# Kernel tuning notes

Measured on AMD Instinct MI355X. Metric: run time of the kernel, lower is better.

Reference implementation:

```python
import jax, jax.numpy as jnp
import numpy as np

EPS = 1e-16


def setup_inputs() -> dict:
    key = jax.random.key(0)
    k1, k2 = jax.random.split(key)
    p = jax.random.normal(k1, (2, 32, 2048, 4), dtype=jnp.float32)
    q = jax.random.normal(k2, (32, 2048, 4), dtype=jnp.float32)
    return {"p": p, "q": q}


def reference(p, q):
    # im=False path: take the real part of the complex generated momenta
    p_real = p[0]                      # (B, N, 4)
    # loss_norm_choice='p3', take_sqrt=True: use 3-momenta (drop energy)
    p3 = p_real[..., 1:]               # (B, N, 3)
    q3 = q[..., 1:]                    # (B, M, 3)
    # Pairwise Euclidean distance (cdist) via the expanded quadratic form to
    # avoid materializing the (B, N, M, 3) difference tensor.
    x2 = jnp.sum(p3 * p3, axis=-1)     # (B, N)
    y2 = jnp.sum(q3 * q3, axis=-1)     # (B, M)
    xy = jnp.einsum('bnd,bmd->bnm', p3, q3)  # (B, N, M)
    dist_sq = x2[..., :, None] + y2[..., None, :] - 2.0 * xy
    dist = jnp.sqrt(jnp.maximum(dist_sq, 0.0) + EPS)  # (B, N, M)
    # Bidirectional nearest-neighbor min-reduction
    min_pq = jnp.min(dist, axis=-1)    # (B, N)
    min_qp = jnp.min(dist, axis=-2)    # (B, M)
    chamfer_loss = jnp.sum((min_pq + min_qp) * 0.5)
    return chamfer_loss
```

## Files before the change

kernel.cpp:

```cpp
#include <hip/hip_runtime.h>
#include <math.h>


#define NPTS   2048
#define NBATCH 32
#define BROWS  128
#define BCOLS  512
#define NBI    (NPTS / BROWS)
#define NJC    (NPTS / BCOLS)
#define WS_ROW_FLOATS ((size_t)NBATCH * NBI * NJC * BROWS)
#define EPSF   1e-16f
#define BIGF   3.4e38f
#define ONEBF  0x3F80u

typedef __attribute__((ext_vector_type(8))) short bf16x8;
typedef __attribute__((ext_vector_type(4))) float f32x4;
typedef __attribute__((ext_vector_type(4))) unsigned int u32x4;

__device__ __forceinline__ float min3f(float a, float b, float c) {
    return fminf(fminf(a, b), c);
}
__device__ __forceinline__ unsigned short bf16_rne(float f) {
    unsigned int u = __float_as_uint(f);
    return (unsigned short)((u + 0x7FFFu + ((u >> 16) & 1u)) >> 16);
}
__device__ __forceinline__ float bf16_f32(unsigned short h) {
    return __uint_as_float(((unsigned int)h) << 16);
}

__global__ __launch_bounds__(256, 4) void chamfer_mfma_kernel(
    const float* __restrict__ P, const float* __restrict__ Q,
    float* __restrict__ ws, float* __restrict__ out)
{
    __shared__ u32x4        sB0[BCOLS];
    __shared__ u32x4        sB1[BCOLS];
    __shared__ u32x4        sB2[BCOLS];
    __shared__ unsigned int scol[BCOLS];
    __shared__ float        srow[BROWS];

    const int tid  = threadIdx.x;
    const int lane = tid & 63;
    const int wv   = tid >> 6;
    const int c15  = lane & 15;
    const int g    = lane >> 4;
    const int bi   = blockIdx.x;
    const int jc   = blockIdx.y;
    const int b    = blockIdx.z;

    if (bi == 0 && jc == 0 && b == 0 && tid == 0) *out = 0.f;

    {
        const float4* Qb = (const float4*)Q + (size_t)b * NPTS + jc * BCOLS;
        #pragma unroll
        for (int s = 0; s < 2; ++s) {
            int c = tid + 256 * s;
            float4 qv = Qb[c];
            float gx = -2.f * qv.y, gy = -2.f * qv.z, gz = -2.f * qv.w;
            unsigned short hx = bf16_rne(gx), hy = bf16_rne(gy), hz = bf16_rne(gz);
            unsigned short lx = bf16_rne(gx - bf16_f32(hx));
            unsigned short ly = bf16_rne(gy - bf16_f32(hy));
            unsigned short lz = bf16_rne(gz - bf16_f32(hz));
            float y2 = fmaf(qv.y, qv.y, fmaf(qv.z, qv.z, qv.w * qv.w));
            unsigned short y2h = bf16_rne(y2);
            unsigned short y2l = bf16_rne(y2 - bf16_f32(y2h));
            sB0[c] = (u32x4){ (unsigned)hx | ((unsigned)hy << 16),
                              (unsigned)hz | ((unsigned)lx << 16),
                              (unsigned)ly | ((unsigned)lz << 16),
                              ONEBF | (ONEBF << 16) };
            sB1[c] = (u32x4){ (unsigned)lx | ((unsigned)ly << 16),
                              (unsigned)lz | ((unsigned)y2h << 16),
                              (unsigned)y2l, 0u };
            sB2[c] = (u32x4){ (unsigned)hx | ((unsigned)hy << 16),
                              (unsigned)hz, 0u, 0u };
            scol[c] = 0x7F7F7F7Fu;
        }
    }

    bf16x8 afrag0, afrag1;
    {
        const float4* Pb = (const float4*)P + (size_t)b * NPTS
                         + bi * BROWS + wv * 32;
        #pragma unroll
        for (int h = 0; h < 2; ++h) {
            float4 pv = Pb[h * 16 + c15];
            float x = pv.y, y = pv.z, z = pv.w;
            unsigned short hx = bf16_rne(x), hy = bf16_rne(y), hz = bf16_rne(z);
            unsigned short lx = bf16_rne(x - bf16_f32(hx));
            unsigned short ly = bf16_rne(y - bf16_f32(hy));
            unsigned short lz = bf16_rne(z - bf16_f32(hz));
            float x2 = fmaf(x, x, fmaf(y, y, z * z));
            unsigned short x2h = bf16_rne(x2);
            unsigned short x2l = bf16_rne(x2 - bf16_f32(x2h));
            u32x4 a;
            if (g == 0)
                a = (u32x4){ (unsigned)hx | ((unsigned)hy << 16),
                             (unsigned)hz | ((unsigned)lx << 16),
                             (unsigned)ly | ((unsigned)lz << 16),
                             (unsigned)x2h | ((unsigned)x2l << 16) };
            else if (g == 1)
                a = (u32x4){ (unsigned)hx | ((unsigned)hy << 16),
                             (unsigned)hz | (ONEBF << 16),
                             ONEBF, 0u };
            else if (g == 2)
                a = (u32x4){ (unsigned)lx | ((unsigned)ly << 16),
                             (unsigned)lz, 0u, 0u };
            else
                a = (u32x4){ 0u, 0u, 0u, 0u };
            if (h == 0) afrag0 = __builtin_bit_cast(bf16x8, a);
            else        afrag1 = __builtin_bit_cast(bf16x8, a);
        }
    }
    __syncthreads();

    const u32x4* bbase = (g == 0) ? sB0 : (g == 1) ? sB1 : sB2;
    const f32x4 cz = {0.f, 0.f, 0.f, 0.f};
    float ra0[4], ra1[4];
    #pragma unroll
    for (int r = 0; r < 4; ++r) { ra0[r] = BIGF; ra1[r] = BIGF; }

    #pragma unroll 2
    for (int t = 0; t < BCOLS / 16; ++t) {
        bf16x8 bfrag = __builtin_bit_cast(bf16x8, bbase[t * 16 + c15]);
        f32x4 d0 = __builtin_amdgcn_mfma_f32_16x16x32_bf16(afrag0, bfrag, cz, 0, 0, 0);
        f32x4 d1 = __builtin_amdgcn_mfma_f32_16x16x32_bf16(afrag1, bfrag, cz, 0, 0, 0);
        #pragma unroll
        for (int r = 0; r < 4; ++r) {
            ra0[r] = fminf(ra0[r], d0[r]);
            ra1[r] = fminf(ra1[r], d1[r]);
        }
        float m = min3f(min3f(d0[0], d0[1], d0[2]),
                        min3f(d0[3], d1[0], d1[1]),
                        fminf(d1[2], d1[3]));
        m = fminf(m, __shfl_xor(m, 16));
        m = fminf(m, __shfl_xor(m, 32));
        if (lane < 16)
            atomicMin(&scol[t * 16 + lane], __float_as_uint(fmaxf(m, 0.f)));
    }

    #pragma unroll
    for (int r = 0; r < 4; ++r) {
        float v0 = ra0[r], v1 = ra1[r];
        v0 = fminf(v0, __shfl_xor(v0, 1)); v1 = fminf(v1, __shfl_xor(v1, 1));
        v0 = fminf(v0, __shfl_xor(v0, 2)); v1 = fminf(v1, __shfl_xor(v1, 2));
        v0 = fminf(v0, __shfl_xor(v0, 4)); v1 = fminf(v1, __shfl_xor(v1, 4));
        v0 = fminf(v0, __shfl_xor(v0, 8)); v1 = fminf(v1, __shfl_xor(v1, 8));
        if (c15 == 0) {
            srow[wv * 32 + g * 4 + r]      = v0;
            srow[wv * 32 + 16 + g * 4 + r] = v1;
        }
    }
    __syncthreads();

    if (tid < BROWS)
        ws[(((size_t)b * NBI + bi) * NJC + jc) * BROWS + tid] = srow[tid];
    {
        float* cb = ws + WS_ROW_FLOATS
                  + (((size_t)b * NJC + jc) * NBI + bi) * BCOLS;
        #pragma unroll
        for (int s = 0; s < 2; ++s) {
            int c = tid + 256 * s;
            cb[c] = __uint_as_float(scol[c]);
        }
    }
}

__global__ __launch_bounds__(256) void chamfer_sum_kernel(
    const float* __restrict__ ws, float* __restrict__ out)
{
    __shared__ float rbuf[4];
    const int tid = threadIdx.x;
    const int i   = blockIdx.x * 256 + tid;
    const int b   = i >> 11;
    const int e   = i & 2047;

    float s;
    {
        const int bi = e >> 7, rl = e & 127;
        const float* rb = ws + ((size_t)(b * NBI + bi) * NJC) * BROWS + rl;
        float v = fminf(fminf(rb[0], rb[BROWS]),
                        fminf(rb[2 * BROWS], rb[3 * BROWS]));
        s = sqrtf(fmaxf(v, 0.f) + EPSF);
    }
    {
        const int jcx = e >> 9, cl = e & 511;
        const float* cb = ws + WS_ROW_FLOATS
                        + ((size_t)(b * NJC + jcx) * NBI) * BCOLS + cl;
        float v = BIGF;
        #pragma unroll
        for (int j = 0; j < NBI; ++j) v = fminf(v, cb[(size_t)j * BCOLS]);
        s += sqrtf(fmaxf(v, 0.f) + EPSF);
    }

    #pragma unroll
    for (int off = 32; off > 0; off >>= 1) s += __shfl_down(s, off);
    if ((tid & 63) == 0) rbuf[tid >> 6] = s;
    __syncthreads();
    if (tid == 0)
        atomicAdd(out, 0.5f * ((rbuf[0] + rbuf[1]) + (rbuf[2] + rbuf[3])));
}

extern "C" void kernel_launch(void* const* d_in, const int* in_sizes, int n_in,
                              void* d_out, int out_size, void* d_ws, size_t ws_size,
                              hipStream_t stream) {
    const float* P = (const float*)d_in[0];
    const float* Q = (const float*)d_in[1];
    float* out = (float*)d_out;
    float* ws  = (float*)d_ws;

    dim3 grid(NBI, NJC, NBATCH);
    chamfer_mfma_kernel<<<grid, 256, 0, stream>>>(P, Q, ws, out);
    chamfer_sum_kernel<<<256, 256, 0, stream>>>(ws, out);
}
```

Before: 80.28 us.

## Fuse final reduction into main kernel via last-block-per-batch counters

```diff
diff --git a/kernel.cpp b/kernel.cpp
--- a/kernel.cpp
+++ b/kernel.cpp
@@ -8,7 +8,9 @@
 #define BCOLS  512
 #define NBI    (NPTS / BROWS)
 #define NJC    (NPTS / BCOLS)
+#define BLKS_PER_BATCH (NBI * NJC)
 #define WS_ROW_FLOATS ((size_t)NBATCH * NBI * NJC * BROWS)
+#define WS_COL_FLOATS ((size_t)NBATCH * NJC * NBI * BCOLS)
 #define EPSF   1e-16f
 #define BIGF   3.4e38f
 #define ONEBF  0x3F80u
@@ -17,6 +19,9 @@
 typedef __attribute__((ext_vector_type(4))) float f32x4;
 typedef __attribute__((ext_vector_type(4))) unsigned int u32x4;
 
+__device__ unsigned int g_cnt[NBATCH];
+__device__ unsigned int g_cnt2;
+
 __device__ __forceinline__ float min3f(float a, float b, float c) {
     return fminf(fminf(a, b), c);
 }
@@ -28,7 +33,7 @@
     return __uint_as_float(((unsigned int)h) << 16);
 }
 
-__global__ __launch_bounds__(256, 4) void chamfer_mfma_kernel(
+__global__ __launch_bounds__(256) void chamfer_mfma_kernel(
     const float* __restrict__ P, const float* __restrict__ Q,
     float* __restrict__ ws, float* __restrict__ out)
 {
@@ -37,6 +42,8 @@
     __shared__ u32x4        sB2[BCOLS];
     __shared__ unsigned int scol[BCOLS];
     __shared__ float        srow[BROWS];
+    __shared__ float        rbuf[4];
+    __shared__ unsigned int sclaim, sfin;
 
     const int tid  = threadIdx.x;
     const int lane = tid & 63;
@@ -46,8 +53,6 @@
     const int bi   = blockIdx.x;
     const int jc   = blockIdx.y;
     const int b    = blockIdx.z;
-
-    if (bi == 0 && jc == 0 && b == 0 && tid == 0) *out = 0.f;
 
     {
         const float4* Qb = (const float4*)Q + (size_t)b * NPTS + jc * BCOLS;
@@ -162,41 +167,58 @@
             cb[c] = __uint_as_float(scol[c]);
         }
     }
-}
-
-__global__ __launch_bounds__(256) void chamfer_sum_kernel(
-    const float* __restrict__ ws, float* __restrict__ out)
-{
-    __shared__ float rbuf[4];
-    const int tid = threadIdx.x;
-    const int i   = blockIdx.x * 256 + tid;
-    const int b   = i >> 11;
-    const int e   = i & 2047;
-
-    float s;
-    {
-        const int bi = e >> 7, rl = e & 127;
-        const float* rb = ws + ((size_t)(b * NBI + bi) * NJC) * BROWS + rl;
-        float v = fminf(fminf(rb[0], rb[BROWS]),
-                        fminf(rb[2 * BROWS], rb[3 * BROWS]));
-        s = sqrtf(fmaxf(v, 0.f) + EPSF);
-    }
-    {
-        const int jcx = e >> 9, cl = e & 511;
-        const float* cb = ws + WS_ROW_FLOATS
-                        + ((size_t)(b * NJC + jcx) * NBI) * BCOLS + cl;
-        float v = BIGF;
-        #pragma unroll
-        for (int j = 0; j < NBI; ++j) v = fminf(v, cb[(size_t)j * BCOLS]);
-        s += sqrtf(fmaxf(v, 0.f) + EPSF);
-    }
-
-    #pragma unroll
-    for (int off = 32; off > 0; off >>= 1) s += __shfl_down(s, off);
-    if ((tid & 63) == 0) rbuf[tid >> 6] = s;
-    __syncthreads();
-    if (tid == 0)
-        atomicAdd(out, 0.5f * ((rbuf[0] + rbuf[1]) + (rbuf[2] + rbuf[3])));
+
+    __threadfence();
+    __syncthreads();
+    if (tid == 0) {
+        unsigned int old = atomicAdd(&g_cnt[b], 1u);
+        sclaim = (old == BLKS_PER_BATCH - 1) ? 1u : 0u;
+        if (sclaim) g_cnt[b] = 0;
+    }
+    __syncthreads();
+    if (sclaim) {
+        __threadfence();
+        float s = 0.f;
+        for (int rr = tid; rr < NPTS; rr += 256) {
+            int rbi = rr >> 7, rl = rr & 127;
+            const float* rb = ws + (((size_t)b * NBI + rbi) * NJC) * BROWS + rl;
+            float v = BIGF;
+            #pragma unroll
+            for (int j = 0; j < NJC; ++j) v = fminf(v, rb[(size_t)j * BROWS]);
+            s += sqrtf(fmaxf(v, 0.f) + EPSF);
+        }
+        for (int cc = tid; cc < NPTS; cc += 256) {
+            int cjc = cc >> 9, cl = cc & 511;
+            const float* cb = ws + WS_ROW_FLOATS
+                            + (((size_t)b * NJC + cjc) * NBI) * BCOLS + cl;
+            float v = BIGF;
+            #pragma unroll
+            for (int j = 0; j < NBI; ++j) v = fminf(v, cb[(size_t)j * BCOLS]);
+            s += sqrtf(fmaxf(v, 0.f) + EPSF);
+        }
+        #pragma unroll
+        for (int off = 32; off > 0; off >>= 1) s += __shfl_down(s, off);
+        if ((tid & 63) == 0) rbuf[tid >> 6] = s;
+        __syncthreads();
+        float* wsum = ws + WS_ROW_FLOATS + WS_COL_FLOATS;
+        if (tid == 0) {
+            wsum[b] = 0.5f * ((rbuf[0] + rbuf[1]) + (rbuf[2] + rbuf[3]));
+            __threadfence();
+            unsigned int old2 = atomicAdd(&g_cnt2, 1u);
+            sfin = (old2 == NBATCH - 1) ? 1u : 0u;
+            if (sfin) g_cnt2 = 0;
+        }
+        __syncthreads();
+        if (sfin) {
+            __threadfence();
+            if (tid < 64) {
+                float v = (tid < NBATCH) ? wsum[tid] : 0.f;
+                #pragma unroll
+                for (int off = 32; off > 0; off >>= 1) v += __shfl_down(v, off);
+                if (tid == 0) *out = v;
+            }
+        }
+    }
 }
 
 extern "C" void kernel_launch(void* const* d_in, const int* in_sizes, int n_in,
@@ -209,5 +231,4 @@
 
     dim3 grid(NBI, NJC, NBATCH);
     chamfer_mfma_kernel<<<grid, 256, 0, stream>>>(P, Q, ws, out);
-    chamfer_sum_kernel<<<256, 256, 0, stream>>>(ws, out);
-}
+}
```

Measured after the change: 262.9 us. 228% more time.
